# Kernel optimization log

Measured on AMD Instinct MI355X. Metric: run time of the kernel, lower is better.

## Reference

```python
import jax, jax.numpy as jnp
import numpy as np

B, S, C, E, H, D, V, K = 1024, 64, 512, 16, 1024, 256, 100, 2
NUM_NUM = 32  # num_numerical; categorical positions are S-NUM_NUM


def setup_inputs() -> dict:
    key = jax.random.key(0)
    ks = jax.random.split(key, 20)
    s = 0.02
    return {
        "codec": jax.random.normal(ks[0], (B, C), jnp.float32),
        "mask_pos": jax.random.randint(ks[1], (B, S), 0, 2, jnp.int32),
        "pos_emb": jax.random.normal(ks[2], (S, C), jnp.float32),
        "type_emb": jax.random.normal(ks[3], (2, C), jnp.float32),
        "gW1": jax.random.normal(ks[4], (3 * C + 1, 256), jnp.float32) * s,
        "gb1": jnp.zeros((256,), jnp.float32),
        "gW2": jax.random.normal(ks[5], (256, E), jnp.float32) * s,
        "gb2": jnp.zeros((E,), jnp.float32),
        "eW0": jax.random.normal(ks[6], (E, C, H), jnp.float32) * s,
        "eb0": jnp.zeros((E, H), jnp.float32),
        "eW1": jax.random.normal(ks[7], (E, H, H), jnp.float32) * s,
        "eb1": jnp.zeros((E, H), jnp.float32),
        "eW2": jax.random.normal(ks[8], (E, H, D), jnp.float32) * s,
        "eb2": jnp.zeros((E, D), jnp.float32),
        "nW": jax.random.normal(ks[9], (NUM_NUM, D), jnp.float32) * s,
        "nb": jnp.zeros((NUM_NUM,), jnp.float32),
        "cW": jax.random.normal(ks[10], (S - NUM_NUM, D, V), jnp.float32) * s,
        "cb": jnp.zeros((S - NUM_NUM, V), jnp.float32),
    }


def reference(codec, mask_pos, pos_emb, type_emb, gW1, gb1, gW2, gb2,
              eW0, eb0, eW1, eb1, eW2, eb2, nW, nb, cW, cb):
    maskf = mask_pos.astype(codec.dtype)  # [B,S]
    positions = jnp.arange(S)
    is_cat = (positions >= NUM_NUM).astype(jnp.int32)
    # gate input: [B,S,3C+1]
    gate_in = jnp.concatenate([
        jnp.broadcast_to(codec[:, None, :], (B, S, C)),
        jnp.broadcast_to(pos_emb[None], (B, S, C)),
        jnp.broadcast_to(type_emb[is_cat][None], (B, S, C)),
        maskf[..., None],
    ], axis=-1)
    h = jax.nn.gelu(gate_in @ gW1 + gb1, approximate=False)
    gate_logits = (h @ gW2 + gb2) * maskf[..., None]  # [B,S,E]
    topg, topi = jax.lax.top_k(gate_logits, K)  # [B,S,K]
    gates = jax.nn.softmax(topg, axis=-1)
    # all expert outputs on codec: [E,B,D]
    h0 = jax.nn.leaky_relu(jnp.einsum('bc,ech->ebh', codec, eW0) + eb0[:, None, :])
    h1 = jax.nn.leaky_relu(jnp.einsum('ebh,ehg->ebg', h0, eW1) + eb1[:, None, :])
    eout = jnp.einsum('ebg,egd->ebd', h1, eW2) + eb2[:, None, :]
    # per-token gather: tok[b,s,k,:] = eout[topi[b,s,k], b, :]
    eout_b = eout.transpose(1, 0, 2)  # [B,E,D]
    tok = jnp.take_along_axis(eout_b[:, None, :, :], topi[..., None], axis=2)  # [B,S,K,D]
    combined = jnp.einsum('bsk,bskd->bsd', gates, tok)  # [B,S,D]
    num_recon = jnp.einsum('bnd,nd->bn', combined[:, :NUM_NUM], nW) + nb  # [B,32]
    cat_recon = jnp.einsum('bnd,ndv->bnv', combined[:, NUM_NUM:], cW) + cb  # [B,32,V]
    return num_recon, cat_recon, gates, topi, mask_pos
```

## Files before the change

### kernel.cpp

```cpp
#include <hip/hip_runtime.h>
#include <hip/hip_bf16.h>

typedef __bf16 bf16x8 __attribute__((ext_vector_type(8)));
typedef float f32x4 __attribute__((ext_vector_type(4)));

static constexpr int B_ = 1024, S_ = 64, C_ = 512, E_ = 16, H_ = 1024, D_ = 256, V_ = 100;
static constexpr int NUMN = 32;

__device__ __forceinline__ unsigned short f2bf(float f) {
  union { float f; unsigned u; } x; x.f = f;
  unsigned r = x.u + 0x7fffu + ((x.u >> 16) & 1u);
  return (unsigned short)(r >> 16);
}

__device__ __forceinline__ float erf_fast(float x) {
  float ax = fabsf(x);
  float t = 1.0f / fmaf(0.3275911f, ax, 1.0f);
  float p = fmaf(1.061405429f, t, -1.453152027f);
  p = fmaf(p, t, 1.421413741f);
  p = fmaf(p, t, -0.284496736f);
  p = fmaf(p, t, 0.254829592f);
  p = p * t;
  float e = 1.0f - p * __expf(-ax * ax);
  return copysignf(e, x);
}

__global__ __launch_bounds__(256) void k_codec_bf(const float* __restrict__ src,
                                                  unsigned short* __restrict__ dst, int n) {
  int i = blockIdx.x * 256 + threadIdx.x;
  if (i < n) dst[i] = f2bf(src[i]);
}

__global__ __launch_bounds__(256) void k_transpose_bf(const float* __restrict__ W,
                                                      unsigned short* __restrict__ WT,
                                                      int K, int N) {
  __shared__ float t[32][33];
  int e = blockIdx.z;
  const float* We = W + (size_t)e * K * N;
  unsigned short* Te = WT + (size_t)e * N * K;
  int n0 = blockIdx.x * 32, k0 = blockIdx.y * 32;
  int tx = threadIdx.x & 31, ty = threadIdx.x >> 5;
#pragma unroll
  for (int i = 0; i < 32; i += 8) t[ty + i][tx] = We[(size_t)(k0 + ty + i) * N + n0 + tx];
  __syncthreads();
#pragma unroll
  for (int i = 0; i < 32; i += 8)
    Te[(size_t)(n0 + ty + i) * K + k0 + tx] = f2bf(t[tx][ty + i]);
}

__global__ __launch_bounds__(256) void k_cwt(const float* __restrict__ cW,
                                             unsigned short* __restrict__ cwt) {
  __shared__ float t[32][33];
  int n = blockIdx.z;
  const float* src = cW + (size_t)n * D_ * V_;
  unsigned short* dst = cwt + (size_t)n * 128 * 256;
  int v0 = blockIdx.x * 32, d0 = blockIdx.y * 32;
  int tx = threadIdx.x & 31, ty = threadIdx.x >> 5;
#pragma unroll
  for (int i = 0; i < 32; i += 8) {
    int v = v0 + tx;
    t[ty + i][tx] = (v < V_) ? src[(size_t)(d0 + ty + i) * V_ + v] : 0.f;
  }
  __syncthreads();
#pragma unroll
  for (int i = 0; i < 32; i += 8)
    dst[(size_t)(v0 + ty + i) * 256 + d0 + tx] = f2bf(t[tx][ty + i]);
}

__global__ __launch_bounds__(256) void k_cvt64(const float* __restrict__ gW2,
                                               const float* __restrict__ gW1,
                                               double* __restrict__ w2d,
                                               double* __restrict__ w1ld,
                                               int* __restrict__ flagcnt) {
  int i = blockIdx.x * 256 + threadIdx.x;
  if (i < 4096) w2d[i] = (double)gW2[i];
  if (i < 256) w1ld[i] = (double)gW1[(size_t)(3 * C_) * 256 + i];
  if (i == 0) *flagcnt = 0;
}

__global__ __launch_bounds__(256) void k_codecpart(const float* __restrict__ codec,
                                                   const float* __restrict__ gW1,
                                                   double* __restrict__ cp) {
  int j = threadIdx.x, b = blockIdx.x;
  const float* cb = codec + (size_t)b * C_;
  double a0 = 0, a1 = 0, a2 = 0, a3 = 0;
  for (int k = 0; k < C_; k += 4) {
    a0 += (double)cb[k] * (double)gW1[(size_t)k * 256 + j];
    a1 += (double)cb[k + 1] * (double)gW1[(size_t)(k + 1) * 256 + j];
    a2 += (double)cb[k + 2] * (double)gW1[(size_t)(k + 2) * 256 + j];
    a3 += (double)cb[k + 3] * (double)gW1[(size_t)(k + 3) * 256 + j];
  }
  cp[(size_t)b * 256 + j] = (a0 + a1) + (a2 + a3);
}

__global__ __launch_bounds__(256) void k_postype_part(const float* __restrict__ pos_emb,
                                                      const float* __restrict__ type_emb,
                                                      const float* __restrict__ gW1,
                                                      double* __restrict__ pp) {
  int j = threadIdx.x;
  int s = blockIdx.x;
  int kc = blockIdx.y;
  int tt = (s >= NUMN) ? 1 : 0;
  double a0 = 0, a1 = 0;
  int k0 = kc * 32;
  for (int kk = 0; kk < 32; kk += 2) {
    int k = k0 + kk;
    a0 += (double)pos_emb[(size_t)s * C_ + k] * (double)gW1[(size_t)(C_ + k) * 256 + j] +
          (double)type_emb[(size_t)tt * C_ + k] * (double)gW1[(size_t)(2 * C_ + k) * 256 + j];
    a1 += (double)pos_emb[(size_t)s * C_ + k + 1] * (double)gW1[(size_t)(C_ + k + 1) * 256 + j] +
          (double)type_emb[(size_t)tt * C_ + k + 1] * (double)gW1[(size_t)(2 * C_ + k + 1) * 256 + j];
  }
  pp[((size_t)kc * 64 + s) * 256 + j] = a0 + a1;
}

__global__ __launch_bounds__(256) void k_postype_red(const double* __restrict__ pp,
                                                     const float* __restrict__ gb1,
                                                     double* __restrict__ ptT) {
  int j = threadIdx.x;
  int s = blockIdx.x;
  double acc = (double)gb1[j];
#pragma unroll
  for (int kc = 0; kc < 16; ++kc) acc += pp[((size_t)kc * 64 + s) * 256 + j];
  ptT[(size_t)j * 64 + s] = acc;
}

__global__ __launch_bounds__(256) void k_gate(const double* __restrict__ cp,
                                              const double* __restrict__ ptT,
                                              const float* __restrict__ gW2,
                                              const double* __restrict__ w1ld,
                                              const float* __restrict__ gb2,
                                              const int* __restrict__ mask,
                                              float* __restrict__ out_g,
                                              float* __restrict__ out_i,
                                              float* __restrict__ out_m,
                                              float* __restrict__ tg,
                                              int* __restrict__ ti,
                                              int* __restrict__ flagcnt,
                                              int* __restrict__ flaglist) {
  __shared__ float red[3][64][17];
  int b = blockIdx.x;
  int s = threadIdx.x & 63;
  int wv = __builtin_amdgcn_readfirstlane(threadIdx.x >> 6);
  int token = b * 64 + s;
  double mf = (double)mask[token];
  const double* cpb = cp + (size_t)b * 256;
  float acc[16];
#pragma unroll
  for (int e = 0; e < 16; ++e) acc[e] = 0.f;
#pragma unroll 2
  for (int jj = 0; jj < 64; ++jj) {
    int j = wv * 64 + jj;
    double xd = cpb[j] + ptT[(size_t)j * 64 + s] + mf * w1ld[j];
    float x = (float)xd;
    float ef = erf_fast(x * 0.70710678f);
    float h = 0.5f * x * (1.0f + ef);
    const float* w2 = gW2 + (size_t)j * 16;
#pragma unroll
    for (int e = 0; e < 16; ++e) acc[e] = fmaf(h, w2[e], acc[e]);
  }
  if (wv > 0) {
#pragma unroll
    for (int e = 0; e < 16; ++e) red[wv - 1][s][e] = acc[e];
  }
  __syncthreads();
  if (wv == 0) {
    double vp[16];
#pragma unroll
    for (int e = 0; e < 16; ++e)
      vp[e] = (double)((acc[e] + red[0][s][e]) + (red[1][s][e] + red[2][s][e])) + (double)gb2[e];
    double margin;
    if (mf == 0.0) {
      double mn = 1e300;
#pragma unroll
      for (int e = 0; e < 16; ++e) mn = fmin(mn, fabs(vp[e]));
      margin = mn;
    } else {
      double t1 = -1e300, t2 = -1e300, t3 = -1e300;
#pragma unroll
      for (int e = 0; e < 16; ++e) {
        double v = vp[e];
        if (v > t1) { t3 = t2; t2 = t1; t1 = v; }
        else if (v > t2) { t3 = t2; t2 = v; }
        else if (v > t3) { t3 = v; }
      }
      margin = fmin(t1 - t2, t2 - t3);
    }
    if (margin < 1e-4) {
      int idx = atomicAdd(flagcnt, 1);
      if (idx < 8192) flaglist[idx] = token;
    }
    double v1, v2;
    int i1, i2;
    if (mf == 0.0) {
      int idx[2];
      int c = 0;
      for (int e = 0; e < 16 && c < 2; ++e)
        if (vp[e] > 0.0) idx[c++] = e;
      for (int e = 0; e < 16 && c < 2; ++e)
        if (!(vp[e] > 0.0)) idx[c++] = e;
      i1 = idx[0];
      i2 = idx[1];
      v1 = 0.0;
      v2 = 0.0;
    } else {
      v1 = -1e300; v2 = -1e300; i1 = 0; i2 = 1;
#pragma unroll
      for (int e = 0; e < 16; ++e) {
        double v = vp[e];
        if (v > v1) { v2 = v1; i2 = i1; v1 = v; i1 = e; }
        else if (v > v2) { v2 = v; i2 = e; }
      }
    }
    double ex = exp(v2 - v1);
    double den = 1.0 + ex;
    float g1 = (float)(1.0 / den), g2 = (float)(ex / den);
    out_g[(size_t)token * 2] = g1;
    out_g[(size_t)token * 2 + 1] = g2;
    out_i[(size_t)token * 2] = (float)i1;
    out_i[(size_t)token * 2 + 1] = (float)i2;
    out_m[token] = (float)mf;
    tg[(size_t)token * 2] = g1;
    tg[(size_t)token * 2 + 1] = g2;
    ti[(size_t)token * 2] = i1;
    ti[(size_t)token * 2 + 1] = i2;
  }
}

__global__ __launch_bounds__(64) void k_gate_fix(const double* __restrict__ cp,
                                                 const double* __restrict__ ptT,
                                                 const double* __restrict__ w2d,
                                                 const double* __restrict__ w1ld,
                                                 const float* __restrict__ gb2,
                                                 const int* __restrict__ mask,
                                                 const int* __restrict__ flagcnt,
                                                 const int* __restrict__ flaglist,
                                                 float* __restrict__ out_g,
                                                 float* __restrict__ out_i,
                                                 float* __restrict__ out_m,
                                                 float* __restrict__ tg,
                                                 int* __restrict__ ti) {
  int cnt = *flagcnt;
  if (cnt > 8192) cnt = 8192;
  int lane = threadIdx.x;
  for (int fi = blockIdx.x; fi < cnt; fi += gridDim.x) {
    int token = flaglist[fi];
    int b = token >> 6, sf = token & 63;
    double mf = (double)mask[token];
    const double* cpb = cp + (size_t)b * 256;
    double facc[16];
#pragma unroll
    for (int e = 0; e < 16; ++e) facc[e] = 0.0;
#pragma unroll
    for (int jj = 0; jj < 4; ++jj) {
      int j = jj * 64 + lane;
      double x = cpb[j] + ptT[(size_t)j * 64 + sf] + mf * w1ld[j];
      double h = 0.5 * x * (1.0 + erf(x * 0.70710678118654752440));
      const double* w2 = w2d + (size_t)j * 16;
#pragma unroll
      for (int e = 0; e < 16; ++e) facc[e] += h * w2[e];
    }
#pragma unroll
    for (int off = 32; off >= 1; off >>= 1) {
#pragma unroll
      for (int e = 0; e < 16; ++e) facc[e] += __shfl_xor(facc[e], off, 64);
    }
    if (lane == 0) {
      double vp[16];
#pragma unroll
      for (int e = 0; e < 16; ++e) vp[e] = facc[e] + (double)gb2[e];
      double v1, v2;
      int i1, i2;
      if (mf == 0.0) {
        int idx[2];
        int c = 0;
        for (int e = 0; e < 16 && c < 2; ++e)
          if (vp[e] > 0.0) idx[c++] = e;
        for (int e = 0; e < 16 && c < 2; ++e)
          if (!(vp[e] > 0.0)) idx[c++] = e;
        i1 = idx[0];
        i2 = idx[1];
        v1 = 0.0;
        v2 = 0.0;
      } else {
        v1 = -1e300; v2 = -1e300; i1 = 0; i2 = 1;
#pragma unroll
        for (int e = 0; e < 16; ++e) {
          double v = vp[e];
          if (v > v1) { v2 = v1; i2 = i1; v1 = v; i1 = e; }
          else if (v > v2) { v2 = v; i2 = e; }
        }
      }
      double ex = exp(v2 - v1);
      double den = 1.0 + ex;
      float g1 = (float)(1.0 / den), g2 = (float)(ex / den);
      out_g[(size_t)token * 2] = g1;
      out_g[(size_t)token * 2 + 1] = g2;
      out_i[(size_t)token * 2] = (float)i1;
      out_i[(size_t)token * 2 + 1] = (float)i2;
      out_m[token] = (float)mf;
      tg[(size_t)token * 2] = g1;
      tg[(size_t)token * 2 + 1] = g2;
      ti[(size_t)token * 2] = i1;
      ti[(size_t)token * 2 + 1] = i2;
    }
  }
}

__global__ __launch_bounds__(512, 2) void k_gemm256(const unsigned short* __restrict__ A, size_t aStride,
                                                    const unsigned short* __restrict__ WT,
                                                    const float* __restrict__ bias,
                                                    unsigned short* __restrict__ Out,
                                                    int M, int N, int K) {
  extern __shared__ char lds[];
  char* sA = lds;
  char* sB = lds + 65536;
  int id = blockIdx.x + gridDim.x * (blockIdx.y + gridDim.y * blockIdx.z);
  int e = (id & 7) * 2 + ((id >> 3) & 1);
  int tile = id >> 4;
  int m0 = (tile & 3) * 256, n0 = (tile >> 2) * 256;
  const unsigned short* Ae = A + (size_t)e * aStride;
  const unsigned short* We = WT + (size_t)e * (size_t)N * K;
  int tid = threadIdx.x, lane = tid & 63, w = tid >> 6;
  int l15 = lane & 15, l4 = lane >> 4;
  int wrow = (w >> 1) * 32;
  int wcol = (w & 1) * 64;
  f32x4 acc[2][2][2][4] = {};
  int nk = K >> 6;

  auto stageA = [&](int buf, int h, int kt) {
#pragma unroll
    for (int c = 0; c < 2; ++c) {
      int off = (tid + c * 512) * 16;
      int row = off >> 7;
      int ss = ((off >> 4) & 7) ^ (row & 7);
      const char* src = (const char*)(Ae + (size_t)(m0 + h * 128 + row) * K + kt * 64) + ss * 16;
      __builtin_amdgcn_global_load_lds((const __attribute__((address_space(1))) void*)src,
          (__attribute__((address_space(3))) void*)(sA + buf * 32768 + h * 16384 + off), 16, 0, 0);
    }
  };
  auto stageB = [&](int buf, int h, int kt) {
#pragma unroll
    for (int c = 0; c < 2; ++c) {
      int off = (tid + c * 512) * 16;
      int row = off >> 7;
      int ss = ((off >> 4) & 7) ^ (row & 7);
      const char* src = (const char*)(We + (size_t)(n0 + h * 128 + row) * K + kt * 64) + ss * 16;
      __builtin_amdgcn_global_load_lds((const __attribute__((address_space(1))) void*)src,
          (__attribute__((address_space(3))) void*)(sB + buf * 32768 + h * 16384 + off), 16, 0, 0);
    }
  };
  auto ldA = [&](int buf, int qm, int mi, int ks) {
    int hrow = wrow + mi * 16 + l15;
    int sp = (l4 + ks * 4) ^ (hrow & 7);
    return *(const bf16x8*)(sA + buf * 32768 + qm * 16384 + hrow * 128 + sp * 16);
  };
  auto ldB = [&](int buf, int qn, int ni, int ks) {
    int hrow = wcol + ni * 16 + l15;
    int sp = (l4 + ks * 4) ^ (hrow & 7);
    return *(const bf16x8*)(sB + buf * 32768 + qn * 16384 + hrow * 128 + sp * 16);
  };

  stageA(0, 0, 0); stageB(0, 0, 0); stageB(0, 1, 0); stageA(0, 1, 0);
  asm volatile("s_waitcnt vmcnt(0)" ::: "memory");
  __builtin_amdgcn_s_barrier();

  bf16x8 a[2][2], b[4][2];
  for (int t = 0; t < nk; ++t) {
    int cur = t & 1, nxt = cur ^ 1;
    bool pf = (t + 1 < nk);
#pragma unroll
    for (int mi = 0; mi < 2; ++mi)
#pragma unroll
      for (int ks = 0; ks < 2; ++ks) a[mi][ks] = ldA(cur, 0, mi, ks);
#pragma unroll
    for (int ni = 0; ni < 4; ++ni)
#pragma unroll
      for (int ks = 0; ks < 2; ++ks) b[ni][ks] = ldB(cur, 0, ni, ks);
    if (pf) stageA(nxt, 0, t + 1);
    __builtin_amdgcn_s_barrier();
    __builtin_amdgcn_s_setprio(1);
#pragma unroll
    for (int mi = 0; mi < 2; ++mi)
#pragma unroll
      for (int ni = 0; ni < 4; ++ni)
#pragma unroll
        for (int ks = 0; ks < 2; ++ks)
          acc[0][0][mi][ni] = __builtin_amdgcn_mfma_f32_16x16x32_bf16(a[mi][ks], b[ni][ks], acc[0][0][mi][ni], 0, 0, 0);
    __builtin_amdgcn_s_setprio(0);
    asm volatile("s_waitcnt vmcnt(4)" ::: "memory");
    __builtin_amdgcn_s_barrier();
#pragma unroll
    for (int ni = 0; ni < 4; ++ni)
#pragma unroll
      for (int ks = 0; ks < 2; ++ks) b[ni][ks] = ldB(cur, 1, ni, ks);
    if (pf) stageB(nxt, 0, t + 1);
    __builtin_amdgcn_s_barrier();
    __builtin_amdgcn_s_setprio(1);
#pragma unroll
    for (int mi = 0; mi < 2; ++mi)
#pragma unroll
      for (int ni = 0; ni < 4; ++ni)
#pragma unroll
        for (int ks = 0; ks < 2; ++ks)
          acc[0][1][mi][ni] = __builtin_amdgcn_mfma_f32_16x16x32_bf16(a[mi][ks], b[ni][ks], acc[0][1][mi][ni], 0, 0, 0);
    __builtin_amdgcn_s_setprio(0);
    asm volatile("s_waitcnt vmcnt(4)" ::: "memory");
    __builtin_amdgcn_s_barrier();
#pragma unroll
    for (int mi = 0; mi < 2; ++mi)
#pragma unroll
      for (int ks = 0; ks < 2; ++ks) a[mi][ks] = ldA(cur, 1, mi, ks);
    if (pf) stageB(nxt, 1, t + 1);
    __builtin_amdgcn_s_barrier();
    __builtin_amdgcn_s_setprio(1);
#pragma unroll
    for (int mi = 0; mi < 2; ++mi)
#pragma unroll
      for (int ni = 0; ni < 4; ++ni)
#pragma unroll
        for (int ks = 0; ks < 2; ++ks)
          acc[1][1][mi][ni] = __builtin_amdgcn_mfma_f32_16x16x32_bf16(a[mi][ks], b[ni][ks], acc[1][1][mi][ni], 0, 0, 0);
    __builtin_amdgcn_s_setprio(0);
    asm volatile("s_waitcnt vmcnt(4)" ::: "memory");
    __builtin_amdgcn_s_barrier();
#pragma unroll
    for (int ni = 0; ni < 4; ++ni)
#pragma unroll
      for (int ks = 0; ks < 2; ++ks) b[ni][ks] = ldB(cur, 0, ni, ks);
    if (pf) stageA(nxt, 1, t + 1);
    __builtin_amdgcn_s_barrier();
    __builtin_amdgcn_s_setprio(1);
#pragma unroll
    for (int mi = 0; mi < 2; ++mi)
#pragma unroll
      for (int ni = 0; ni < 4; ++ni)
#pragma unroll
        for (int ks = 0; ks < 2; ++ks)
          acc[1][0][mi][ni] = __builtin_amdgcn_mfma_f32_16x16x32_bf16(a[mi][ks], b[ni][ks], acc[1][0][mi][ni], 0, 0, 0);
    __builtin_amdgcn_s_setprio(0);
    asm volatile("s_waitcnt vmcnt(4)" ::: "memory");
    __builtin_amdgcn_s_barrier();
  }

  size_t obase = (size_t)e * (size_t)M * N;
#pragma unroll
  for (int qm = 0; qm < 2; ++qm)
#pragma unroll
    for (int qn = 0; qn < 2; ++qn)
#pragma unroll
      for (int mi = 0; mi < 2; ++mi)
#pragma unroll
        for (int ni = 0; ni < 4; ++ni) {
          int col = n0 + qn * 128 + wcol + ni * 16 + l15;
          float bv = bias[(size_t)e * N + col];
#pragma unroll
          for (int j = 0; j < 4; ++j) {
            int row = m0 + qm * 128 + wrow + mi * 16 + l4 * 4 + j;
            float v = acc[qm][qn][mi][ni][j] + bv;
            v = (v > 0.f) ? v : 0.01f * v;
            Out[obase + (size_t)row * N + col] = f2bf(v);
          }
        }
}

template <int ACT, int OBF>
__global__ __launch_bounds__(256) void k_gemm(const unsigned short* __restrict__ A, size_t aStride,
                                              const unsigned short* __restrict__ WT,
                                              const float* __restrict__ bias,
                                              void* __restrict__ Out,
                                              int M, int N, int K) {
  __shared__ __align__(16) unsigned short sA[128 * 32];
  __shared__ __align__(16) unsigned short sB[128 * 32];
  int e = blockIdx.z;
  int m0 = blockIdx.x * 128, n0 = blockIdx.y * 128;
  const unsigned short* Ae = A + (size_t)e * aStride;
  const unsigned short* We = WT + (size_t)e * (size_t)N * K;
  int tid = threadIdx.x, lane = tid & 63, w = tid >> 6;
  int l15 = lane & 15, kh = (lane >> 4) * 8;
  int rsub = lane >> 2;
  int kk = (lane & 3) * 8;
  int wr = (w >> 1) * 64, wc = (w & 1) * 64;
  f32x4 acc[4][4] = {};
  int nk = K >> 5;

  auto stage = [&](int kt) {
#pragma unroll
    for (int c = 0; c < 2; ++c) {
      int chunk = w * 2 + c;
      int row = chunk * 16 + rsub;
      const unsigned short* ga = Ae + (size_t)(m0 + row) * K + kt * 32 + kk;
      __builtin_amdgcn_global_load_lds((const __attribute__((address_space(1))) void*)ga,
                                       (__attribute__((address_space(3))) void*)(&sA[chunk * 512]),
                                       16, 0, 0);
      const unsigned short* gb = We + (size_t)(n0 + row) * K + kt * 32 + kk;
      __builtin_amdgcn_global_load_lds((const __attribute__((address_space(1))) void*)gb,
                                       (__attribute__((address_space(3))) void*)(&sB[chunk * 512]),
                                       16, 0, 0);
    }
  };

  stage(0);
  for (int kt = 0; kt < nk; ++kt) {
    __syncthreads();
    bf16x8 a[4], bb[4];
#pragma unroll
    for (int mi = 0; mi < 4; ++mi)
      a[mi] = *(const bf16x8*)&sA[(wr + mi * 16 + l15) * 32 + kh];
#pragma unroll
    for (int ni = 0; ni < 4; ++ni)
      bb[ni] = *(const bf16x8*)&sB[(wc + ni * 16 + l15) * 32 + kh];
#pragma unroll
    for (int mi = 0; mi < 4; ++mi)
#pragma unroll
      for (int ni = 0; ni < 4; ++ni)
        acc[mi][ni] = __builtin_amdgcn_mfma_f32_16x16x32_bf16(a[mi], bb[ni], acc[mi][ni], 0, 0, 0);
    if (kt + 1 < nk) {
      __syncthreads();
      stage(kt + 1);
    }
  }

  unsigned short* outb = (unsigned short*)Out;
  float* outf = (float*)Out;
  size_t obase = (size_t)e * (size_t)M * N;
#pragma unroll
  for (int mi = 0; mi < 4; ++mi) {
#pragma unroll
    for (int ni = 0; ni < 4; ++ni) {
      int col = n0 + wc + ni * 16 + l15;
      float bv = bias[(size_t)e * N + col];
#pragma unroll
      for (int j = 0; j < 4; ++j) {
        int row = m0 + wr + mi * 16 + (lane >> 4) * 4 + j;
        float v = acc[mi][ni][j] + bv;
        if (ACT) v = (v > 0.f) ? v : 0.01f * v;
        if (OBF) outb[obase + (size_t)row * N + col] = f2bf(v);
        else outf[obase + (size_t)row * N + col] = v;
      }
    }
  }
}

__global__ __launch_bounds__(256) void k_comb(const float* __restrict__ eout,
                                              const float* __restrict__ tg,
                                              const int* __restrict__ ti,
                                              unsigned short* __restrict__ combbf) {
  int b = blockIdx.x, n = blockIdx.y, d = threadIdx.x;
  int tk = b * 64 + 32 + n;
  float g1 = tg[(size_t)tk * 2], g2 = tg[(size_t)tk * 2 + 1];
  int i1 = ti[(size_t)tk * 2], i2 = ti[(size_t)tk * 2 + 1];
  float v = g1 * eout[((size_t)i1 * B_ + b) * D_ + d] + g2 * eout[((size_t)i2 * B_ + b) * D_ + d];
  combbf[((size_t)n * B_ + b) * D_ + d] = f2bf(v);
}

__global__ __launch_bounds__(256) void k_catgemm(const unsigned short* __restrict__ combbf,
                                                 const unsigned short* __restrict__ cwt,
                                                 const float* __restrict__ cb,
                                                 float* __restrict__ out1) {
  __shared__ __align__(16) unsigned short sA[128 * 32];
  __shared__ __align__(16) unsigned short sB[128 * 32];
  int n = blockIdx.z;
  int m0 = blockIdx.x * 128;
  const unsigned short* Ae = combbf + (size_t)n * B_ * D_;
  const unsigned short* We = cwt + (size_t)n * 128 * 256;
  int tid = threadIdx.x, lane = tid & 63, w = tid >> 6;
  int l15 = lane & 15, kh = (lane >> 4) * 8;
  int rsub = lane >> 2;
  int kk = (lane & 3) * 8;
  int wr = (w >> 1) * 64, wc = (w & 1) * 64;
  f32x4 acc[4][4] = {};
  const int K = 256, nk = K >> 5;

  auto stage = [&](int kt) {
#pragma unroll
    for (int c = 0; c < 2; ++c) {
      int chunk = w * 2 + c;
      int row = chunk * 16 + rsub;
      const unsigned short* ga = Ae + (size_t)(m0 + row) * K + kt * 32 + kk;
      __builtin_amdgcn_global_load_lds((const __attribute__((address_space(1))) void*)ga,
                                       (__attribute__((address_space(3))) void*)(&sA[chunk * 512]),
                                       16, 0, 0);
      const unsigned short* gb = We + (size_t)row * K + kt * 32 + kk;
      __builtin_amdgcn_global_load_lds((const __attribute__((address_space(1))) void*)gb,
                                       (__attribute__((address_space(3))) void*)(&sB[chunk * 512]),
                                       16, 0, 0);
    }
  };

  stage(0);
  for (int kt = 0; kt < nk; ++kt) {
    __syncthreads();
    bf16x8 a[4], bb[4];
#pragma unroll
    for (int mi = 0; mi < 4; ++mi)
      a[mi] = *(const bf16x8*)&sA[(wr + mi * 16 + l15) * 32 + kh];
#pragma unroll
    for (int ni = 0; ni < 4; ++ni)
      bb[ni] = *(const bf16x8*)&sB[(wc + ni * 16 + l15) * 32 + kh];
#pragma unroll
    for (int mi = 0; mi < 4; ++mi)
#pragma unroll
      for (int ni = 0; ni < 4; ++ni)
        acc[mi][ni] = __builtin_amdgcn_mfma_f32_16x16x32_bf16(a[mi], bb[ni], acc[mi][ni], 0, 0, 0);
    if (kt + 1 < nk) {
      __syncthreads();
      stage(kt + 1);
    }
  }

#pragma unroll
  for (int mi = 0; mi < 4; ++mi) {
#pragma unroll
    for (int ni = 0; ni < 4; ++ni) {
      int col = wc + ni * 16 + l15;
      if (col < V_) {
        float bv = cb[(size_t)n * V_ + col];
#pragma unroll
        for (int j = 0; j < 4; ++j) {
          int row = m0 + wr + mi * 16 + (lane >> 4) * 4 + j;
          out1[((size_t)row * 32 + n) * V_ + col] = acc[mi][ni][j] + bv;
        }
      }
    }
  }
}

__global__ __launch_bounds__(256) void k_num(const float* __restrict__ eout,
                                             const float* __restrict__ nW,
                                             const float* __restrict__ nb,
                                             const float* __restrict__ tg,
                                             const int* __restrict__ ti,
                                             float* __restrict__ out0) {
  int b = blockIdx.x;
  int lane = threadIdx.x & 63;
  int wv = threadIdx.x >> 6;
#pragma unroll
  for (int q = 0; q < 8; ++q) {
    int n = wv * 8 + q;
    int tk = b * 64 + n;
    float g1 = tg[(size_t)tk * 2], g2 = tg[(size_t)tk * 2 + 1];
    int i1 = ti[(size_t)tk * 2], i2 = ti[(size_t)tk * 2 + 1];
    const float4* p1 = (const float4*)(eout + ((size_t)i1 * B_ + b) * D_);
    const float4* p2 = (const float4*)(eout + ((size_t)i2 * B_ + b) * D_);
    const float4* wp = (const float4*)(nW + (size_t)n * D_);
    float4 a = p1[lane], c = p2[lane], ww = wp[lane];
    float acc = fmaf(g1, a.x, g2 * c.x) * ww.x + fmaf(g1, a.y, g2 * c.y) * ww.y +
                fmaf(g1, a.z, g2 * c.z) * ww.z + fmaf(g1, a.w, g2 * c.w) * ww.w;
#pragma unroll
    for (int off = 32; off >= 1; off >>= 1) acc += __shfl_xor(acc, off, 64);
    if (lane == 0) out0[(size_t)b * 32 + n] = nb[n] + acc;
  }
}

extern "C" void kernel_launch(void* const* d_in, const int* in_sizes, int n_in,
                              void* d_out, int out_size, void* d_ws, size_t ws_size,
                              hipStream_t stream) {
  const float* codec = (const float*)d_in[0];
  const int* maskp = (const int*)d_in[1];
  const float* pos_emb = (const float*)d_in[2];
  const float* type_emb = (const float*)d_in[3];
  const float* gW1 = (const float*)d_in[4];
  const float* gb1 = (const float*)d_in[5];
  const float* gW2 = (const float*)d_in[6];
  const float* gb2 = (const float*)d_in[7];
  const float* eW0 = (const float*)d_in[8];
  const float* eb0 = (const float*)d_in[9];
  const float* eW1 = (const float*)d_in[10];
  const float* eb1 = (const float*)d_in[11];
  const float* eW2 = (const float*)d_in[12];
  const float* eb2 = (const float*)d_in[13];
  const float* nW = (const float*)d_in[14];
  const float* nb = (const float*)d_in[15];
  const float* cW = (const float*)d_in[16];
  const float* cb = (const float*)d_in[17];

  char* ws = (char*)d_ws;
  size_t o = 0;
  unsigned short* codecbf = (unsigned short*)(ws + o); o += (size_t)B_ * C_ * 2;
  size_t o_w0t = o;
  unsigned short* w0t = (unsigned short*)(ws + o); o += (size_t)E_ * H_ * C_ * 2;
  unsigned short* w1t = (unsigned short*)(ws + o); o += (size_t)E_ * H_ * H_ * 2;
  unsigned short* w2t = (unsigned short*)(ws + o); o += (size_t)E_ * D_ * H_ * 2;
  size_t o_h0 = o;
  unsigned short* h0 = (unsigned short*)(ws + o); o += (size_t)E_ * B_ * H_ * 2;
  unsigned short* h1 = (unsigned short*)(ws + o); o += (size_t)E_ * B_ * H_ * 2;
  double* cp = (double*)(ws + o); o += (size_t)B_ * 256 * 8;
  double* ptT = (double*)(ws + o); o += (size_t)S_ * 256 * 8;
  float* tg = (float*)(ws + o); o += (size_t)B_ * S_ * 2 * 4;
  int* ti = (int*)(ws + o); o += (size_t)B_ * S_ * 2 * 4;
  double* w2d = (double*)(ws + o); o += 4096 * 8;
  double* w1ld = (double*)(ws + o); o += 256 * 8;
  unsigned short* cwt = (unsigned short*)(ws + o); o += (size_t)32 * 128 * 256 * 2;
  double* pp = (double*)(ws + o); o += (size_t)16 * 64 * 256 * 8;
  int* flagcnt = (int*)(ws + o); o += 256;
  int* flaglist = (int*)(ws + o); o += 8192 * 4;
  float* eout = (float*)(ws + o_w0t);
  unsigned short* combbf = (unsigned short*)(ws + o_h0);

  float* out = (float*)d_out;
  float* out_num = out;
  float* out_cat = out + 32768;
  float* out_g = out + 32768 + 3276800;
  float* out_i = out_g + (size_t)B_ * S_ * 2;
  float* out_m = out_i + (size_t)B_ * S_ * 2;

  hipLaunchKernelGGL(k_codec_bf, dim3((B_ * C_) / 256), dim3(256), 0, stream, codec, codecbf, B_ * C_);
  hipLaunchKernelGGL(k_cvt64, dim3(16), dim3(256), 0, stream, gW2, gW1, w2d, w1ld, flagcnt);
  hipLaunchKernelGGL(k_transpose_bf, dim3(H_ / 32, C_ / 32, E_), dim3(256), 0, stream, eW0, w0t, C_, H_);
  hipLaunchKernelGGL(k_transpose_bf, dim3(H_ / 32, H_ / 32, E_), dim3(256), 0, stream, eW1, w1t, H_, H_);
  hipLaunchKernelGGL(k_transpose_bf, dim3(D_ / 32, H_ / 32, E_), dim3(256), 0, stream, eW2, w2t, H_, D_);
  hipLaunchKernelGGL(k_cwt, dim3(4, 8, 32), dim3(256), 0, stream, cW, cwt);
  hipLaunchKernelGGL(k_codecpart, dim3(B_), dim3(256), 0, stream, codec, gW1, cp);
  hipLaunchKernelGGL(k_postype_part, dim3(S_, 16), dim3(256), 0, stream, pos_emb, type_emb, gW1, pp);
  hipLaunchKernelGGL(k_postype_red, dim3(S_), dim3(256), 0, stream, pp, gb1, ptT);
  hipLaunchKernelGGL(k_gate, dim3(B_), dim3(256), 0, stream, cp, ptT, gW2, w1ld, gb2,
                     maskp, out_g, out_i, out_m, tg, ti, flagcnt, flaglist);
  hipLaunchKernelGGL(k_gate_fix, dim3(2048), dim3(64), 0, stream, cp, ptT, w2d, w1ld, gb2,
                     maskp, flagcnt, flaglist, out_g, out_i, out_m, tg, ti);
  hipLaunchKernelGGL(k_gemm256, dim3(4, 4, E_), dim3(512), 131072, stream,
                     codecbf, (size_t)0, w0t, eb0, h0, 1024, 1024, 512);
  hipLaunchKernelGGL(k_gemm256, dim3(4, 4, E_), dim3(512), 131072, stream,
                     h0, (size_t)(B_ * H_), w1t, eb1, h1, 1024, 1024, 1024);
  hipLaunchKernelGGL((k_gemm<0, 0>), dim3(8, 2, E_), dim3(256), 0, stream,
                     h1, (size_t)(B_ * H_), w2t, eb2, (void*)eout, 1024, 256, 1024);
  hipLaunchKernelGGL(k_comb, dim3(B_, 32), dim3(256), 0, stream, eout, tg, ti, combbf);
  hipLaunchKernelGGL(k_num, dim3(B_), dim3(256), 0, stream, eout, nW, nb, tg, ti, out_num);
  hipLaunchKernelGGL(k_catgemm, dim3(8, 1, 32), dim3(256), 0, stream, combbf, cwt, cb, out_cat);
}
```

Baseline: 233.6 us.

## Restructure 256x256 GEMM to 2x4 warp layout with single-barrier double buffering

Result: no change. 230.0 us (-1.5%).

```diff
diff --git a/kernel.cpp b/kernel.cpp
--- a/kernel.cpp
+++ b/kernel.cpp
@@ -322,9 +322,11 @@
   const unsigned short* We = WT + (size_t)e * (size_t)N * K;
   int tid = threadIdx.x, lane = tid & 63, w = tid >> 6;
   int l15 = lane & 15, l4 = lane >> 4;
-  int wrow = (w >> 1) * 32;
-  int wcol = (w & 1) * 64;
-  f32x4 acc[2][2][2][4] = {};
+  int r = w >> 2;
+  int cc = (w & 3) * 64;
+  int hc = cc >> 7;
+  int cr = cc & 127;
+  f32x4 acc[2][4][4] = {};
   int nk = K >> 6;
 
   auto stageA = [&](int buf, int h, int kt) {
@@ -349,118 +351,67 @@
           (__attribute__((address_space(3))) void*)(sB + buf * 32768 + h * 16384 + off), 16, 0, 0);
     }
   };
-  auto ldA = [&](int buf, int qm, int mi, int ks) {
-    int hrow = wrow + mi * 16 + l15;
+  auto ldA = [&](int buf, int m2, int mi, int ks) {
+    int hrow = m2 * 64 + mi * 16 + l15;
     int sp = (l4 + ks * 4) ^ (hrow & 7);
-    return *(const bf16x8*)(sA + buf * 32768 + qm * 16384 + hrow * 128 + sp * 16);
+    return *(const bf16x8*)(sA + buf * 32768 + r * 16384 + hrow * 128 + sp * 16);
   };
-  auto ldB = [&](int buf, int qn, int ni, int ks) {
-    int hrow = wcol + ni * 16 + l15;
+  auto ldB = [&](int buf, int ni, int ks) {
+    int hrow = cr + ni * 16 + l15;
     int sp = (l4 + ks * 4) ^ (hrow & 7);
-    return *(const bf16x8*)(sB + buf * 32768 + qn * 16384 + hrow * 128 + sp * 16);
+    return *(const bf16x8*)(sB + buf * 32768 + hc * 16384 + hrow * 128 + sp * 16);
   };
 
-  stageA(0, 0, 0); stageB(0, 0, 0); stageB(0, 1, 0); stageA(0, 1, 0);
+  stageA(0, 0, 0); stageA(0, 1, 0); stageB(0, 0, 0); stageB(0, 1, 0);
   asm volatile("s_waitcnt vmcnt(0)" ::: "memory");
   __builtin_amdgcn_s_barrier();
 
-  bf16x8 a[2][2], b[4][2];
   for (int t = 0; t < nk; ++t) {
     int cur = t & 1, nxt = cur ^ 1;
-    bool pf = (t + 1 < nk);
-#pragma unroll
-    for (int mi = 0; mi < 2; ++mi)
-#pragma unroll
-      for (int ks = 0; ks < 2; ++ks) a[mi][ks] = ldA(cur, 0, mi, ks);
-#pragma unroll
-    for (int ni = 0; ni < 4; ++ni)
-#pragma unroll
-      for (int ks = 0; ks < 2; ++ks) b[ni][ks] = ldB(cur, 0, ni, ks);
-    if (pf) stageA(nxt, 0, t + 1);
+    if (t + 1 < nk) {
+      stageA(nxt, 0, t + 1); stageA(nxt, 1, t + 1);
+      stageB(nxt, 0, t + 1); stageB(nxt, 1, t + 1);
+    }
+#pragma unroll
+    for (int ks = 0; ks < 2; ++ks) {
+      bf16x8 bfr[4];
+#pragma unroll
+      for (int ni = 0; ni < 4; ++ni) bfr[ni] = ldB(cur, ni, ks);
+#pragma unroll
+      for (int m2 = 0; m2 < 2; ++m2) {
+        bf16x8 afr[4];
+#pragma unroll
+        for (int mi = 0; mi < 4; ++mi) afr[mi] = ldA(cur, m2, mi, ks);
+        __builtin_amdgcn_s_setprio(1);
+#pragma unroll
+        for (int mi = 0; mi < 4; ++mi)
+#pragma unroll
+          for (int ni = 0; ni < 4; ++ni)
+            acc[m2][mi][ni] = __builtin_amdgcn_mfma_f32_16x16x32_bf16(afr[mi], bfr[ni], acc[m2][mi][ni], 0, 0, 0);
+        __builtin_amdgcn_s_setprio(0);
+      }
+    }
+    asm volatile("s_waitcnt vmcnt(0)" ::: "memory");
     __builtin_amdgcn_s_barrier();
-    __builtin_amdgcn_s_setprio(1);
-#pragma unroll
-    for (int mi = 0; mi < 2; ++mi)
-#pragma unroll
-      for (int ni = 0; ni < 4; ++ni)
-#pragma unroll
-        for (int ks = 0; ks < 2; ++ks)
-          acc[0][0][mi][ni] = __builtin_amdgcn_mfma_f32_16x16x32_bf16(a[mi][ks], b[ni][ks], acc[0][0][mi][ni], 0, 0, 0);
-    __builtin_amdgcn_s_setprio(0);
-    asm volatile("s_waitcnt vmcnt(4)" ::: "memory");
-    __builtin_amdgcn_s_barrier();
-#pragma unroll
-    for (int ni = 0; ni < 4; ++ni)
-#pragma unroll
-      for (int ks = 0; ks < 2; ++ks) b[ni][ks] = ldB(cur, 1, ni, ks);
-    if (pf) stageB(nxt, 0, t + 1);
-    __builtin_amdgcn_s_barrier();
-    __builtin_amdgcn_s_setprio(1);
-#pragma unroll
-    for (int mi = 0; mi < 2; ++mi)
-#pragma unroll
-      for (int ni = 0; ni < 4; ++ni)
-#pragma unroll
-        for (int ks = 0; ks < 2; ++ks)
-          acc[0][1][mi][ni] = __builtin_amdgcn_mfma_f32_16x16x32_bf16(a[mi][ks], b[ni][ks], acc[0][1][mi][ni], 0, 0, 0);
-    __builtin_amdgcn_s_setprio(0);
-    asm volatile("s_waitcnt vmcnt(4)" ::: "memory");
-    __builtin_amdgcn_s_barrier();
-#pragma unroll
-    for (int mi = 0; mi < 2; ++mi)
-#pragma unroll
-      for (int ks = 0; ks < 2; ++ks) a[mi][ks] = ldA(cur, 1, mi, ks);
-    if (pf) stageB(nxt, 1, t + 1);
-    __builtin_amdgcn_s_barrier();
-    __builtin_amdgcn_s_setprio(1);
-#pragma unroll
-    for (int mi = 0; mi < 2; ++mi)
-#pragma unroll
-      for (int ni = 0; ni < 4; ++ni)
-#pragma unroll
-        for (int ks = 0; ks < 2; ++ks)
-          acc[1][1][mi][ni] = __builtin_amdgcn_mfma_f32_16x16x32_bf16(a[mi][ks], b[ni][ks], acc[1][1][mi][ni], 0, 0, 0);
-    __builtin_amdgcn_s_setprio(0);
-    asm volatile("s_waitcnt vmcnt(4)" ::: "memory");
-    __builtin_amdgcn_s_barrier();
-#pragma unroll
-    for (int ni = 0; ni < 4; ++ni)
-#pragma unroll
-      for (int ks = 0; ks < 2; ++ks) b[ni][ks] = ldB(cur, 0, ni, ks);
-    if (pf) stageA(nxt, 1, t + 1);
-    __builtin_amdgcn_s_barrier();
-    __builtin_amdgcn_s_setprio(1);
-#pragma unroll
-    for (int mi = 0; mi < 2; ++mi)
-#pragma unroll
-      for (int ni = 0; ni < 4; ++ni)
-#pragma unroll
-        for (int ks = 0; ks < 2; ++ks)
-          acc[1][0][mi][ni] = __builtin_amdgcn_mfma_f32_16x16x32_bf16(a[mi][ks], b[ni][ks], acc[1][0][mi][ni], 0, 0, 0);
-    __builtin_amdgcn_s_setprio(0);
-    asm volatile("s_waitcnt vmcnt(4)" ::: "memory");
-    __builtin_amdgcn_s_barrier();
   }
 
   size_t obase = (size_t)e * (size_t)M * N;
 #pragma unroll
-  for (int qm = 0; qm < 2; ++qm)
-#pragma unroll
-    for (int qn = 0; qn < 2; ++qn)
-#pragma unroll
-      for (int mi = 0; mi < 2; ++mi)
-#pragma unroll
-        for (int ni = 0; ni < 4; ++ni) {
-          int col = n0 + qn * 128 + wcol + ni * 16 + l15;
-          float bv = bias[(size_t)e * N + col];
-#pragma unroll
-          for (int j = 0; j < 4; ++j) {
-            int row = m0 + qm * 128 + wrow + mi * 16 + l4 * 4 + j;
-            float v = acc[qm][qn][mi][ni][j] + bv;
-            v = (v > 0.f) ? v : 0.01f * v;
-            Out[obase + (size_t)row * N + col] = f2bf(v);
-          }
+  for (int m2 = 0; m2 < 2; ++m2)
+#pragma unroll
+    for (int mi = 0; mi < 4; ++mi)
+#pragma unroll
+      for (int ni = 0; ni < 4; ++ni) {
+        int col = n0 + cc + ni * 16 + l15;
+        float bv = bias[(size_t)e * N + col];
+#pragma unroll
+        for (int j = 0; j < 4; ++j) {
+          int row = m0 + r * 128 + m2 * 64 + mi * 16 + l4 * 4 + j;
+          float v = acc[m2][mi][ni][j] + bv;
+          v = (v > 0.f) ? v : 0.01f * v;
+          Out[obase + (size_t)row * N + col] = f2bf(v);
         }
+      }
 }
 
 template <int ACT, int OBF>
```
